# Optimization experiments

Hardware: AMD Instinct MI355X
Metric: run time of the kernel (lower is better)

Reference implementation:

```python
import jax, jax.numpy as jnp
import numpy as np

B, D, Nh, L = 8, 128, 8, 1024
Dk = D // Nh  # 16
Dv = D // Nh  # 16

def _xavier(key, shape):
    # nn.init.xavier_normal_ on a 3D tensor treats dim0 as fan irrelevant:
    # fan_in = shape[-1]*1, fan_out = shape[-2]*1 for >=2D; receptive field = prod(shape[2:])? For 3D torch uses
    # fan_in = shape[1]*shape[2]? We just need same distribution family; use std from last two dims.
    fan_in, fan_out = shape[-1], shape[-2]
    std = float(np.sqrt(2.0 / (fan_in + fan_out)))
    return jax.random.normal(key, shape, dtype=jnp.float32) * std

def setup_inputs() -> dict:
    key = jax.random.key(0)
    kx, kq, kk, kv, ko = jax.random.split(key, 5)
    x = jax.random.normal(kx, (B, D, L), dtype=jnp.float32)
    Wq = _xavier(kq, (Nh, B, Dk, D))
    Wk = _xavier(kk, (Nh, B, Dk, D))
    Wv = _xavier(kv, (Nh, B, Dv, D))
    Wo = _xavier(ko, (B, Dv * Nh, D))
    return {"x": x, "Wq": Wq, "Wk": Wk, "Wv": Wv, "Wo": Wo}

def reference(x, Wq, Wk, Wv, Wo):
    scale = 1.0 / np.sqrt(Dk)
    # Project all heads at once: [Nh,B,Dk,D] x [B,D,L] -> [B,Nh,Dk,L]
    Q = jnp.einsum('hbkd,bdl->bhkl', Wq, x)
    K = jnp.einsum('hbkd,bdl->bhkl', Wk, x)
    V = jnp.einsum('hbvd,bdl->bhvl', Wv, x)
    # scores[b,h,i,j] = sum_k Q[b,h,k,i] * K[b,h,k,j]
    scores = jnp.einsum('bhki,bhkj->bhij', Q, K) * scale
    # original softmaxes over dim=1 of [B,L,L] -> the i (Q-length) axis
    attn = jax.nn.softmax(scores, axis=2)
    # head[b,h,v,j] = sum_i V[b,h,v,i] * attn[b,h,i,j]
    head = jnp.einsum('bhvi,bhij->bhvj', V, attn)
    # concat heads along channel dim (order matches torch.cat over head list)
    head = head.reshape(B, Nh * Dv, L)
    # Wo [B, Nh*Dv, D] bmm head [B, D(=Nh*Dv), L] -> [B, Nh*Dv, L]
    out = jnp.einsum('bod,bdl->bol', Wo, head)
    return out
```

## Files before the change

### kernel.cpp

```cpp
#include <hip/hip_runtime.h>
#include <hip/hip_bf16.h>

#define B_ 8
#define D_ 128
#define NH 8
#define L_ 1024
#define DK 16

typedef __attribute__((ext_vector_type(4))) short s4;
typedef __attribute__((ext_vector_type(4))) float f4;

static __device__ __forceinline__ unsigned short f2bf(float f) {
    __hip_bfloat16 h = __float2bfloat16(f);
    return *reinterpret_cast<unsigned short*>(&h);
}
static __device__ __forceinline__ unsigned pack2(float a, float b) {
    return (unsigned)f2bf(a) | ((unsigned)f2bf(b) << 16);
}
static __device__ __forceinline__ s4 pack4(float a, float b, float c, float d) {
    union { unsigned u[2]; s4 v; } un;
    un.u[0] = pack2(a, b);
    un.u[1] = pack2(c, d);
    return un.v;
}

#if __has_builtin(__builtin_amdgcn_mfma_f32_16x16x16_bf16)
#define MFMA16(a, b, c) __builtin_amdgcn_mfma_f32_16x16x16_bf16(a, b, c, 0, 0, 0)
#elif __has_builtin(__builtin_amdgcn_mfma_f32_16x16x16bf16_1k)
#define MFMA16(a, b, c) __builtin_amdgcn_mfma_f32_16x16x16bf16_1k(a, b, c, 0, 0, 0)
#else
static __device__ __forceinline__ f4 mfma16_asm(s4 a, s4 b, f4 c) {
    f4 d;
    asm volatile("v_mfma_f32_16x16x16_bf16 %0, %1, %2, %3"
                 : "=&v"(d) : "v"(a), "v"(b), "v"(c));
    return d;
}
#define MFMA16(a, b, c) mfma16_asm(a, b, c)
#endif

__global__ __launch_bounds__(256)
void proj_kernel(const float* __restrict__ x,
                 const float* __restrict__ Wq,
                 const float* __restrict__ Wk,
                 const float* __restrict__ Wv,
                 unsigned short* __restrict__ Qt,
                 unsigned short* __restrict__ Kt,
                 unsigned short* __restrict__ Vt) {
    const int lane = threadIdx.x & 63;
    const int wv   = threadIdx.x >> 6;
    const int m = lane & 15, q = lane >> 4;
    const int bh = blockIdx.y, b = bh >> 3, h = bh & 7;
    const int which = blockIdx.z;
    const int n0 = (blockIdx.x * 4 + wv) * 32;

    const float* W = (which == 0) ? Wq : (which == 1) ? Wk : Wv;
    const float* Wrow = W + ((size_t)((h * B_ + b) * DK + m)) * D_;
    const float* xb = x + (size_t)b * D_ * L_ + n0 + m;

    f4 acc0 = {0.f, 0.f, 0.f, 0.f}, acc1 = {0.f, 0.f, 0.f, 0.f};
#pragma unroll
    for (int kb = 0; kb < 8; ++kb) {
        const int k4 = kb * 16 + q * 4;
        float4 wf = *(const float4*)(Wrow + k4);
        s4 a = pack4(wf.x, wf.y, wf.z, wf.w);

        const float* xc = xb + (size_t)k4 * L_;
        float b00 = xc[0];          float b01 = xc[L_];
        float b02 = xc[2 * L_];     float b03 = xc[3 * L_];
        float b10 = xc[16];         float b11 = xc[L_ + 16];
        float b12 = xc[2 * L_ + 16];float b13 = xc[3 * L_ + 16];
        s4 bf0 = pack4(b00, b01, b02, b03);
        s4 bf1 = pack4(b10, b11, b12, b13);

        acc0 = MFMA16(a, bf0, acc0);
        acc1 = MFMA16(a, bf1, acc1);
    }

    if (which == 2) {
        unsigned short* vp = Vt + ((size_t)bh * DK + q * 4) * L_ + n0 + m;
        vp[0]      = f2bf(acc0[0]); vp[L_]     = f2bf(acc0[1]);
        vp[2 * L_] = f2bf(acc0[2]); vp[3 * L_] = f2bf(acc0[3]);
        vp += 16;
        vp[0]      = f2bf(acc1[0]); vp[L_]     = f2bf(acc1[1]);
        vp[2 * L_] = f2bf(acc1[2]); vp[3 * L_] = f2bf(acc1[3]);
    } else {
        const float sc = (which == 1) ? 0.25f : 1.0f;
        unsigned short* T = (which == 0) ? Qt : Kt;
        uint2 u0, u1;
        u0.x = pack2(acc0[0] * sc, acc0[1] * sc);
        u0.y = pack2(acc0[2] * sc, acc0[3] * sc);
        u1.x = pack2(acc1[0] * sc, acc1[1] * sc);
        u1.y = pack2(acc1[2] * sc, acc1[3] * sc);
        *(uint2*)(T + ((size_t)bh * L_ + n0 + m) * DK + q * 4)      = u0;
        *(uint2*)(T + ((size_t)bh * L_ + n0 + 16 + m) * DK + q * 4) = u1;
    }
}

__global__ __launch_bounds__(256)
void attn_out_kernel(const unsigned short* __restrict__ Qt,
                     const unsigned short* __restrict__ Kt,
                     const unsigned short* __restrict__ Vt,
                     const float* __restrict__ Wo,
                     float* __restrict__ out) {
    const int lane = threadIdx.x & 63;
    const int wv   = threadIdx.x >> 6;
    const int m = lane & 15, q = lane >> 4;
    const int b    = blockIdx.y;
    const int jblk = blockIdx.x * 32;

    __shared__ unsigned short hls[32][132];

#pragma unroll
    for (int hh = 0; hh < 2; ++hh) {
        const int h  = wv + hh * 4;
        const int bh = b * NH + h;

        s4 bk0 = *(const s4*)(Kt + ((size_t)bh * L_ + jblk + m) * DK + q * 4);
        s4 bk1 = *(const s4*)(Kt + ((size_t)bh * L_ + jblk + 16 + m) * DK + q * 4);

        f4 O0 = {0.f, 0.f, 0.f, 0.f}, O1 = {0.f, 0.f, 0.f, 0.f};
        float ls0 = 0.f, ls1 = 0.f;
        const unsigned short* qbase = Qt + (size_t)bh * L_ * DK + q * 4;
        const unsigned short* vbase = Vt + ((size_t)bh * DK + m) * L_ + q * 4;

#pragma unroll 4
        for (int i0 = 0; i0 < L_; i0 += 16) {
            s4 aq = *(const s4*)(qbase + (size_t)(i0 + m) * DK);
            s4 av = *(const s4*)(vbase + i0);

            f4 z = {0.f, 0.f, 0.f, 0.f};
            f4 S0 = MFMA16(aq, bk0, z);
            f4 S1 = MFMA16(aq, bk1, z);

            float p00 = __expf(S0[0]), p01 = __expf(S0[1]);
            float p02 = __expf(S0[2]), p03 = __expf(S0[3]);
            float p10 = __expf(S1[0]), p11 = __expf(S1[1]);
            float p12 = __expf(S1[2]), p13 = __expf(S1[3]);
            ls0 += (p00 + p01) + (p02 + p03);
            ls1 += (p10 + p11) + (p12 + p13);

            s4 pb0, pb1;
            pb0[0] = (short)f2bf(p00); pb0[1] = (short)f2bf(p01);
            pb0[2] = (short)f2bf(p02); pb0[3] = (short)f2bf(p03);
            pb1[0] = (short)f2bf(p10); pb1[1] = (short)f2bf(p11);
            pb1[2] = (short)f2bf(p12); pb1[3] = (short)f2bf(p13);

            O0 = MFMA16(av, pb0, O0);
            O1 = MFMA16(av, pb1, O1);
        }

        ls0 += __shfl_xor(ls0, 16, 64);
        ls0 += __shfl_xor(ls0, 32, 64);
        ls1 += __shfl_xor(ls1, 16, 64);
        ls1 += __shfl_xor(ls1, 32, 64);
        const float inv0 = 1.f / ls0, inv1 = 1.f / ls1;

        uint2 o0, o1;
        o0.x = pack2(O0[0] * inv0, O0[1] * inv0);
        o0.y = pack2(O0[2] * inv0, O0[3] * inv0);
        o1.x = pack2(O1[0] * inv1, O1[1] * inv1);
        o1.y = pack2(O1[2] * inv1, O1[3] * inv1);
        *(uint2*)&hls[m][h * 16 + q * 4]      = o0;
        *(uint2*)&hls[16 + m][h * 16 + q * 4] = o1;
    }

    __syncthreads();

#pragma unroll
    for (int t = 0; t < 2; ++t) {
        const int oc = wv * 2 + t;
        const int o0 = oc * 16;
        const float* Wrow = Wo + ((size_t)b * D_ + o0 + m) * D_;

        f4 acc0 = {0.f, 0.f, 0.f, 0.f}, acc1 = {0.f, 0.f, 0.f, 0.f};
#pragma unroll
        for (int kb = 0; kb < 8; ++kb) {
            const int k4 = kb * 16 + q * 4;
            float4 wf = *(const float4*)(Wrow + k4);
            s4 a  = pack4(wf.x, wf.y, wf.z, wf.w);
            s4 b0 = *(const s4*)&hls[m][k4];
            s4 b1 = *(const s4*)&hls[16 + m][k4];
            acc0 = MFMA16(a, b0, acc0);
            acc1 = MFMA16(a, b1, acc1);
        }

        float* op = out + ((size_t)b * D_ + o0 + q * 4) * L_ + jblk + m;
        op[0]      = acc0[0]; op[L_]     = acc0[1];
        op[2 * L_] = acc0[2]; op[3 * L_] = acc0[3];
        op += 16;
        op[0]      = acc1[0]; op[L_]     = acc1[1];
        op[2 * L_] = acc1[2]; op[3 * L_] = acc1[3];
    }
}

extern "C" void kernel_launch(void* const* d_in, const int* in_sizes, int n_in,
                              void* d_out, int out_size, void* d_ws, size_t ws_size,
                              hipStream_t stream) {
    const float* x  = (const float*)d_in[0];
    const float* Wq = (const float*)d_in[1];
    const float* Wk = (const float*)d_in[2];
    const float* Wv = (const float*)d_in[3];
    const float* Wo = (const float*)d_in[4];
    float* out = (float*)d_out;

    const size_t SEG = (size_t)B_ * NH * DK * L_;
    unsigned short* Qt = (unsigned short*)d_ws;
    unsigned short* Kt = Qt + SEG;
    unsigned short* Vt = Kt + SEG;

    proj_kernel<<<dim3(8, B_ * NH, 3), 256, 0, stream>>>(x, Wq, Wk, Wv, Qt, Kt, Vt);
    attn_out_kernel<<<dim3(32, B_), 256, 0, stream>>>(Qt, Kt, Vt, Wo, out);
}
```

Before: 103.6 us.

## Fuse projection and attention into one cooperative kernel with grid sync

Merges the QKV projection kernel and the attention+output-projection kernel into a single cooperative launch of 256 blocks. The blocks first grid-stride over the projection tiles, then synchronise the whole grid before running the attention stage. This removes one kernel launch and the gap between kernels. In exchange it adds a grid-wide barrier and the overhead of a cooperative launch, and the projection stage now runs on fewer blocks that each loop over several tiles.

```diff
diff --git a/kernel.cpp b/kernel.cpp
--- a/kernel.cpp
+++ b/kernel.cpp
@@ -1,5 +1,6 @@
 #include <hip/hip_runtime.h>
 #include <hip/hip_bf16.h>
+#include <hip/hip_cooperative_groups.h>
 
 #define B_ 8
 #define D_ 128
@@ -39,74 +40,74 @@
 #endif
 
 __global__ __launch_bounds__(256)
-void proj_kernel(const float* __restrict__ x,
-                 const float* __restrict__ Wq,
-                 const float* __restrict__ Wk,
-                 const float* __restrict__ Wv,
-                 unsigned short* __restrict__ Qt,
-                 unsigned short* __restrict__ Kt,
-                 unsigned short* __restrict__ Vt) {
+void fused_kernel(const float* __restrict__ x,
+                  const float* __restrict__ Wq,
+                  const float* __restrict__ Wk,
+                  const float* __restrict__ Wv,
+                  const float* __restrict__ Wo,
+                  unsigned short* __restrict__ Qt,
+                  unsigned short* __restrict__ Kt,
+                  unsigned short* __restrict__ Vt,
+                  float* __restrict__ out) {
     const int lane = threadIdx.x & 63;
     const int wv   = threadIdx.x >> 6;
     const int m = lane & 15, q = lane >> 4;
-    const int bh = blockIdx.y, b = bh >> 3, h = bh & 7;
-    const int which = blockIdx.z;
-    const int n0 = (blockIdx.x * 4 + wv) * 32;
-
-    const float* W = (which == 0) ? Wq : (which == 1) ? Wk : Wv;
-    const float* Wrow = W + ((size_t)((h * B_ + b) * DK + m)) * D_;
-    const float* xb = x + (size_t)b * D_ * L_ + n0 + m;
-
-    f4 acc0 = {0.f, 0.f, 0.f, 0.f}, acc1 = {0.f, 0.f, 0.f, 0.f};
-#pragma unroll
-    for (int kb = 0; kb < 8; ++kb) {
-        const int k4 = kb * 16 + q * 4;
-        float4 wf = *(const float4*)(Wrow + k4);
-        s4 a = pack4(wf.x, wf.y, wf.z, wf.w);
-
-        const float* xc = xb + (size_t)k4 * L_;
-        float b00 = xc[0];          float b01 = xc[L_];
-        float b02 = xc[2 * L_];     float b03 = xc[3 * L_];
-        float b10 = xc[16];         float b11 = xc[L_ + 16];
-        float b12 = xc[2 * L_ + 16];float b13 = xc[3 * L_ + 16];
-        s4 bf0 = pack4(b00, b01, b02, b03);
-        s4 bf1 = pack4(b10, b11, b12, b13);
-
-        acc0 = MFMA16(a, bf0, acc0);
-        acc1 = MFMA16(a, bf1, acc1);
+
+    const int w = blockIdx.x * 4 + wv;
+    for (int t = w; t < 6144; t += 1024) {
+        const int n0    = (t & 31) * 32;
+        const int bh    = (t >> 5) & 63;
+        const int which = t >> 11;
+        const int b = bh >> 3, h = bh & 7;
+
+        const float* W = (which == 0) ? Wq : (which == 1) ? Wk : Wv;
+        const float* Wrow = W + ((size_t)((h * B_ + b) * DK + m)) * D_;
+        const float* xb = x + (size_t)b * D_ * L_ + n0 + m;
+
+        f4 acc0 = {0.f, 0.f, 0.f, 0.f}, acc1 = {0.f, 0.f, 0.f, 0.f};
+#pragma unroll
+        for (int kb = 0; kb < 8; ++kb) {
+            const int k4 = kb * 16 + q * 4;
+            float4 wf = *(const float4*)(Wrow + k4);
+            s4 a = pack4(wf.x, wf.y, wf.z, wf.w);
+
+            const float* xc = xb + (size_t)k4 * L_;
+            float b00 = xc[0];           float b01 = xc[L_];
+            float b02 = xc[2 * L_];      float b03 = xc[3 * L_];
+            float b10 = xc[16];          float b11 = xc[L_ + 16];
+            float b12 = xc[2 * L_ + 16]; float b13 = xc[3 * L_ + 16];
+            s4 bf0 = pack4(b00, b01, b02, b03);
+            s4 bf1 = pack4(b10, b11, b12, b13);
+
+            acc0 = MFMA16(a, bf0, acc0);
+            acc1 = MFMA16(a, bf1, acc1);
+        }
+
+        if (which == 2) {
+            unsigned short* vp = Vt + ((size_t)bh * DK + q * 4) * L_ + n0 + m;
+            vp[0]      = f2bf(acc0[0]); vp[L_]     = f2bf(acc0[1]);
+            vp[2 * L_] = f2bf(acc0[2]); vp[3 * L_] = f2bf(acc0[3]);
+            vp += 16;
+            vp[0]      = f2bf(acc1[0]); vp[L_]     = f2bf(acc1[1]);
+            vp[2 * L_] = f2bf(acc1[2]); vp[3 * L_] = f2bf(acc1[3]);
+        } else {
+            const float sc = (which == 1) ? 0.25f : 1.0f;
+            unsigned short* T = (which == 0) ? Qt : Kt;
+            uint2 u0, u1;
+            u0.x = pack2(acc0[0] * sc, acc0[1] * sc);
+            u0.y = pack2(acc0[2] * sc, acc0[3] * sc);
+            u1.x = pack2(acc1[0] * sc, acc1[1] * sc);
+            u1.y = pack2(acc1[2] * sc, acc1[3] * sc);
+            *(uint2*)(T + ((size_t)bh * L_ + n0 + m) * DK + q * 4)      = u0;
+            *(uint2*)(T + ((size_t)bh * L_ + n0 + 16 + m) * DK + q * 4) = u1;
+        }
     }
 
-    if (which == 2) {
-        unsigned short* vp = Vt + ((size_t)bh * DK + q * 4) * L_ + n0 + m;
-        vp[0]      = f2bf(acc0[0]); vp[L_]     = f2bf(acc0[1]);
-        vp[2 * L_] = f2bf(acc0[2]); vp[3 * L_] = f2bf(acc0[3]);
-        vp += 16;
-        vp[0]      = f2bf(acc1[0]); vp[L_]     = f2bf(acc1[1]);
-        vp[2 * L_] = f2bf(acc1[2]); vp[3 * L_] = f2bf(acc1[3]);
-    } else {
-        const float sc = (which == 1) ? 0.25f : 1.0f;
-        unsigned short* T = (which == 0) ? Qt : Kt;
-        uint2 u0, u1;
-        u0.x = pack2(acc0[0] * sc, acc0[1] * sc);
-        u0.y = pack2(acc0[2] * sc, acc0[3] * sc);
-        u1.x = pack2(acc1[0] * sc, acc1[1] * sc);
-        u1.y = pack2(acc1[2] * sc, acc1[3] * sc);
-        *(uint2*)(T + ((size_t)bh * L_ + n0 + m) * DK + q * 4)      = u0;
-        *(uint2*)(T + ((size_t)bh * L_ + n0 + 16 + m) * DK + q * 4) = u1;
-    }
-}
-
-__global__ __launch_bounds__(256)
-void attn_out_kernel(const unsigned short* __restrict__ Qt,
-                     const unsigned short* __restrict__ Kt,
-                     const unsigned short* __restrict__ Vt,
-                     const float* __restrict__ Wo,
-                     float* __restrict__ out) {
-    const int lane = threadIdx.x & 63;
-    const int wv   = threadIdx.x >> 6;
-    const int m = lane & 15, q = lane >> 4;
-    const int b    = blockIdx.y;
-    const int jblk = blockIdx.x * 32;
+    __threadfence();
+    cooperative_groups::this_grid().sync();
+
+    const int b    = blockIdx.x >> 5;
+    const int jblk = (blockIdx.x & 31) * 32;
 
     __shared__ unsigned short hls[32][132];
 
@@ -208,6 +209,8 @@
     unsigned short* Kt = Qt + SEG;
     unsigned short* Vt = Kt + SEG;
 
-    proj_kernel<<<dim3(8, B_ * NH, 3), 256, 0, stream>>>(x, Wq, Wk, Wv, Qt, Kt, Vt);
-    attn_out_kernel<<<dim3(32, B_), 256, 0, stream>>>(Qt, Kt, Vt, Wo, out);
-}
+    void* args[] = {(void*)&x, (void*)&Wq, (void*)&Wk, (void*)&Wv, (void*)&Wo,
+                    (void*)&Qt, (void*)&Kt, (void*)&Vt, (void*)&out};
+    hipLaunchCooperativeKernel((const void*)fused_kernel,
+                               dim3(256), dim3(256), args, 0, stream);
+}
```

Result: slower. 179.0 us (+72.8%).
